# Kernel optimization log

Hardware: AMD Instinct MI355X
Metric: run time of the kernel (lower is better)

The kernel has to match this reference:

```python
import jax, jax.numpy as jnp
import numpy as np

NH, NKV, HD = 16, 8, 128  # heads, kv heads, head dim
N_REP = NH // NKV
EPS = 1e-06
K_MASK = float(jnp.finfo(jnp.bfloat16).min)
SCALE = HD ** -0.5


def _rms_norm(x, w):
    xf = x.astype(jnp.float32)
    rms = jnp.sqrt(jnp.mean(xf * xf, axis=-1, keepdims=True) + EPS)
    return (xf / rms * w).astype(x.dtype)


def _rotate_half(x):
    x1, x2 = jnp.split(x, 2, axis=-1)
    return jnp.concatenate([-x2, x1], axis=-1)


def setup_inputs() -> dict:
    key = jax.random.key(0)
    ks = jax.random.split(key, 5)
    B, S, H = 1, 2048, 2048
    hidden_states = jax.random.normal(ks[0], (B, S, H), jnp.float32)
    # real RoPE tables (duplicated-half layout), theta = 5e6
    pos = jnp.arange(S, dtype=jnp.float32)
    inv_freq = 1.0 / (5_000_000.0 ** (jnp.arange(0, HD, 2, dtype=jnp.float32) / HD))
    ang = pos[:, None] * inv_freq[None, :]            # (S, HD/2)
    emb = jnp.concatenate([ang, ang], axis=-1)[None]  # (1, S, HD)
    cos, sin = jnp.cos(emb), jnp.sin(emb)
    attention_mask = jnp.tril(jnp.ones((S, S), bool))[None, None]  # causal (1,1,S,S)
    sc = 0.02
    wq = jax.random.normal(ks[1], (H, NH * HD), jnp.float32) * sc
    wk = jax.random.normal(ks[2], (H, NKV * HD), jnp.float32) * sc
    wv = jax.random.normal(ks[3], (H, NKV * HD), jnp.float32) * sc
    wo = jax.random.normal(ks[4], (NH * HD, H), jnp.float32) * sc
    q_norm_w = jnp.ones((HD,), jnp.float32)
    k_norm_w = jnp.ones((HD,), jnp.float32)
    return {"hidden_states": hidden_states, "cos": cos, "sin": sin,
            "attention_mask": attention_mask, "wq": wq, "wk": wk, "wv": wv,
            "wo": wo, "q_norm_w": q_norm_w, "k_norm_w": k_norm_w}


def reference(hidden_states, cos, sin, attention_mask, wq, wk, wv, wo, q_norm_w, k_norm_w):
    B, S, H = hidden_states.shape
    q = (hidden_states @ wq).reshape(B, S, NH, HD)
    k = (hidden_states @ wk).reshape(B, S, NKV, HD)
    v = (hidden_states @ wv).reshape(B, S, NKV, HD)
    q = _rms_norm(q, q_norm_w)
    k = _rms_norm(k, k_norm_w)
    c = cos[:, :, None, :]
    s = sin[:, :, None, :]
    q = q * c + _rotate_half(q) * s
    k = k * c + _rotate_half(k) * s
    # GQA: group q heads by kv head; same math as jnp.repeat + matmul
    qg = q.reshape(B, S, NKV, N_REP, HD)
    scores = jnp.einsum('bqgrd,bkgd->bgrqk', qg, k) * SCALE  # (B,NKV,N_REP,S,S)
    scores = jnp.where(attention_mask[:, :, None], scores, K_MASK)
    attn = jax.nn.softmax(scores.astype(jnp.float32), axis=-1).astype(q.dtype)
    out = jnp.einsum('bgrqk,bkgd->bqgrd', attn, v)            # (B,S,NKV,N_REP,HD)
    out = out.reshape(B, S, NH * HD)
    return out @ wo
```

## Files before the change

### kernel.cpp

```cpp
#include <hip/hip_runtime.h>
#include <hip/hip_bf16.h>
#include <stdint.h>

typedef _Float16 half8 __attribute__((ext_vector_type(8)));
typedef _Float16 half4 __attribute__((ext_vector_type(4)));
typedef float f32x4 __attribute__((ext_vector_type(4)));

#define MFMA16(A, B, C) __builtin_amdgcn_mfma_f32_16x16x32_f16(A, B, C, 0, 0, 0)

static constexpr int Sdim = 2048;
static constexpr int NH = 16;
static constexpr int NKV = 8;
static constexpr int HD = 128;
static constexpr float ATT_SCALE = 0.08838834764831845f;
static constexpr float S0 = 4.0f;

__device__ __forceinline__ void async_copy16(const _Float16* g, _Float16* l) {
  auto gp = reinterpret_cast<const __attribute__((address_space(1))) uint32_t*>(
      reinterpret_cast<uintptr_t>(g));
  auto lp = reinterpret_cast<__attribute__((address_space(3))) uint32_t*>(
      reinterpret_cast<uintptr_t>(l));
  __builtin_amdgcn_global_load_lds(gp, lp, 16, 0, 0);
}

__global__ __launch_bounds__(256) void xconv(const float* __restrict__ X,
                                             _Float16* __restrict__ Xh) {
  int i = (blockIdx.x * 256 + threadIdx.x) * 4;
  float4 v = *(const float4*)(X + i);
  half4 h = {(_Float16)v.x, (_Float16)v.y, (_Float16)v.z, (_Float16)v.w};
  *(half4*)(Xh + i) = h;
}

__global__ __launch_bounds__(256) void wtrans_all(const float* __restrict__ wq,
                                                  const float* __restrict__ wk,
                                                  const float* __restrict__ wv,
                                                  const float* __restrict__ wo,
                                                  _Float16* __restrict__ wqT,
                                                  _Float16* __restrict__ wkT,
                                                  _Float16* __restrict__ wvT,
                                                  _Float16* __restrict__ woT) {
  const float* W;
  _Float16* WT;
  int N;
  switch (blockIdx.z) {
    case 0: W = wq; WT = wqT; N = 2048; break;
    case 1: W = wk; WT = wkT; N = 1024; break;
    case 2: W = wv; WT = wvT; N = 1024; break;
    default: W = wo; WT = woT; N = 2048; break;
  }
  if ((int)blockIdx.x * 64 >= N) return;
  const int K = 2048;
  __shared__ __align__(16) float tile[64][68];
  int n0 = blockIdx.x * 64, k0 = blockIdx.y * 64;
  int t = threadIdx.x;
  int c = (t & 15) * 4;
  int rb = t >> 4;
  for (int p = 0; p < 4; ++p) {
    int k = p * 16 + rb;
    *(float4*)&tile[k][c] = *(const float4*)(W + (size_t)(k0 + k) * N + n0 + c);
  }
  __syncthreads();
  int n = t >> 2;
  int kc = (t & 3) * 16;
  half8 o0, o1;
  for (int i = 0; i < 8; ++i) {
    o0[i] = (_Float16)tile[kc + i][n];
    o1[i] = (_Float16)tile[kc + 8 + i][n];
  }
  _Float16* dst = WT + (size_t)(n0 + n) * K + k0 + kc;
  *(half8*)dst = o0;
  *(half8*)(dst + 8) = o1;
}

template <int NI>
__device__ __forceinline__ void stage64(const _Float16* __restrict__ src, size_t stride,
                                        int k0, _Float16* lds, int w, int lane) {
  for (int ii = 0; ii < NI; ++ii) {
    int i = w * NI + ii;
    int row = i * 8 + (lane >> 3);
    int c = (lane & 7) ^ (row & 7);
    async_copy16(src + (size_t)row * stride + k0 + c * 8, lds + i * 512);
  }
}

__device__ __forceinline__ int frag_off(int row, int ks, int quad, int col) {
  return row * 64 + (((ks << 2) | quad) ^ (col & 7)) * 8;
}

__global__ __launch_bounds__(256, 2) void gemm_qkv(const _Float16* __restrict__ Xh,
                                                   const _Float16* __restrict__ wqT,
                                                   const _Float16* __restrict__ wkT,
                                                   const _Float16* __restrict__ wvT,
                                                   _Float16* __restrict__ Q,
                                                   _Float16* __restrict__ K,
                                                   _Float16* __restrict__ Vt) {
  __shared__ __align__(16) _Float16 As[2][128 * 64];
  __shared__ __align__(16) _Float16 Bs[2][128 * 64];
  int bx = blockIdx.x, m0 = blockIdx.y * 128;
  const _Float16* BT;
  _Float16* outp;
  int n0, Nst;
  bool vt;
  if (bx < 16)      { BT = wqT; outp = Q;  n0 = bx * 128;        vt = false; Nst = 2048; }
  else if (bx < 24) { BT = wkT; outp = K;  n0 = (bx - 16) * 128; vt = false; Nst = 1024; }
  else              { BT = wvT; outp = Vt; n0 = (bx - 24) * 128; vt = true;  Nst = 2048; }
  int t = threadIdx.x, lane = t & 63, w = t >> 6;
  int col = lane & 15, quad = lane >> 4;
  int wm = (w & 1) * 64, wn = (w >> 1) * 64;
  const _Float16* Ap = Xh + (size_t)m0 * 2048;
  const _Float16* Bp = BT + (size_t)n0 * 2048;
  f32x4 acc[4][4] = {};
  stage64<4>(Ap, 2048, 0, As[0], w, lane);
  stage64<4>(Bp, 2048, 0, Bs[0], w, lane);
#pragma unroll 1
  for (int it = 0; it < 32; ++it) {
    int c = it & 1;
    if (it + 1 < 32) {
      stage64<4>(Ap, 2048, (it + 1) * 64, As[c ^ 1], w, lane);
      stage64<4>(Bp, 2048, (it + 1) * 64, Bs[c ^ 1], w, lane);
      asm volatile("s_waitcnt vmcnt(8)" ::: "memory");
    } else {
      asm volatile("s_waitcnt vmcnt(0)" ::: "memory");
    }
    __builtin_amdgcn_sched_barrier(0);
    __builtin_amdgcn_s_barrier();
    __builtin_amdgcn_sched_barrier(0);
    half8 af[4][2], bf[4][2];
    for (int i = 0; i < 4; ++i)
      for (int ks = 0; ks < 2; ++ks) {
        af[i][ks] = *(const half8*)(As[c] + frag_off(wm + i * 16 + col, ks, quad, col));
        bf[i][ks] = *(const half8*)(Bs[c] + frag_off(wn + i * 16 + col, ks, quad, col));
      }
    __builtin_amdgcn_s_setprio(1);
    if (!vt) {
      for (int ks = 0; ks < 2; ++ks)
        for (int i = 0; i < 4; ++i)
          for (int j = 0; j < 4; ++j)
            acc[i][j] = MFMA16(bf[j][ks], af[i][ks], acc[i][j]);
    } else {
      for (int ks = 0; ks < 2; ++ks)
        for (int i = 0; i < 4; ++i)
          for (int j = 0; j < 4; ++j)
            acc[i][j] = MFMA16(af[i][ks], bf[j][ks], acc[i][j]);
    }
    __builtin_amdgcn_s_setprio(0);
    __builtin_amdgcn_sched_barrier(0);
    __builtin_amdgcn_s_barrier();
    __builtin_amdgcn_sched_barrier(0);
  }
  if (!vt) {
    for (int i = 0; i < 4; ++i)
      for (int j = 0; j < 4; ++j) {
        int m = m0 + wm + i * 16 + col;
        int n = n0 + wn + j * 16 + quad * 4;
        half4 hv = {(_Float16)acc[i][j][0], (_Float16)acc[i][j][1],
                    (_Float16)acc[i][j][2], (_Float16)acc[i][j][3]};
        *(half4*)(outp + (size_t)m * Nst + n) = hv;
      }
  } else {
    for (int i = 0; i < 4; ++i)
      for (int j = 0; j < 4; ++j) {
        int n = n0 + wn + j * 16 + col;
        int mb = m0 + wm + i * 16 + quad * 4;
        half4 hv = {(_Float16)acc[i][j][0], (_Float16)acc[i][j][1],
                    (_Float16)acc[i][j][2], (_Float16)acc[i][j][3]};
        *(half4*)(outp + (size_t)n * Sdim + mb) = hv;
      }
  }
}

__global__ __launch_bounds__(256, 2) void gemm_o(const _Float16* __restrict__ A,
                                                 const _Float16* __restrict__ BT,
                                                 float* __restrict__ C) {
  __shared__ __align__(16) _Float16 As[2][64 * 64];
  __shared__ __align__(16) _Float16 Bs[2][128 * 64];
  int m0 = blockIdx.y * 64, n0 = blockIdx.x * 128;
  int t = threadIdx.x, lane = t & 63, w = t >> 6;
  int col = lane & 15, quad = lane >> 4;
  int wm = (w & 1) * 32, wn = (w >> 1) * 64;
  const _Float16* Ap = A + (size_t)m0 * 2048;
  const _Float16* Bp = BT + (size_t)n0 * 2048;
  f32x4 acc[2][4] = {};
  stage64<2>(Ap, 2048, 0, As[0], w, lane);
  stage64<4>(Bp, 2048, 0, Bs[0], w, lane);
#pragma unroll 1
  for (int it = 0; it < 32; ++it) {
    int c = it & 1;
    if (it + 1 < 32) {
      stage64<2>(Ap, 2048, (it + 1) * 64, As[c ^ 1], w, lane);
      stage64<4>(Bp, 2048, (it + 1) * 64, Bs[c ^ 1], w, lane);
      asm volatile("s_waitcnt vmcnt(6)" ::: "memory");
    } else {
      asm volatile("s_waitcnt vmcnt(0)" ::: "memory");
    }
    __builtin_amdgcn_sched_barrier(0);
    __builtin_amdgcn_s_barrier();
    __builtin_amdgcn_sched_barrier(0);
    half8 af[2][2], bf[4][2];
    for (int ks = 0; ks < 2; ++ks) {
      for (int i = 0; i < 2; ++i)
        af[i][ks] = *(const half8*)(As[c] + frag_off(wm + i * 16 + col, ks, quad, col));
      for (int j = 0; j < 4; ++j)
        bf[j][ks] = *(const half8*)(Bs[c] + frag_off(wn + j * 16 + col, ks, quad, col));
    }
    __builtin_amdgcn_s_setprio(1);
    for (int ks = 0; ks < 2; ++ks)
      for (int i = 0; i < 2; ++i)
        for (int j = 0; j < 4; ++j)
          acc[i][j] = MFMA16(bf[j][ks], af[i][ks], acc[i][j]);
    __builtin_amdgcn_s_setprio(0);
    __builtin_amdgcn_sched_barrier(0);
    __builtin_amdgcn_s_barrier();
    __builtin_amdgcn_sched_barrier(0);
  }
  for (int i = 0; i < 2; ++i)
    for (int j = 0; j < 4; ++j) {
      int m = m0 + wm + i * 16 + col;
      int n = n0 + wn + j * 16 + quad * 4;
      *(f32x4*)(C + (size_t)m * 2048 + n) = acc[i][j];
    }
}

__global__ __launch_bounds__(256) void rmsrope_all(const _Float16* __restrict__ Qraw,
                                                   const _Float16* __restrict__ Kraw,
                                                   _Float16* __restrict__ Qn,
                                                   _Float16* __restrict__ Kn,
                                                   const float* __restrict__ cs,
                                                   const float* __restrict__ sn,
                                                   const float* __restrict__ qw,
                                                   const float* __restrict__ kw) {
  int w = threadIdx.x >> 6, lane = threadIdx.x & 63;
  int gw = blockIdx.x * 4 + w;
  const _Float16* src;
  _Float16* dst;
  const float* nw;
  int m, h, nh;
  float scale;
  if (gw < Sdim * NH) {
    m = gw >> 4; h = gw & 15; nh = NH; src = Qraw; dst = Qn; nw = qw; scale = ATT_SCALE;
  } else {
    int g2 = gw - Sdim * NH;
    m = g2 >> 3; h = g2 & 7; nh = NKV; src = Kraw; dst = Kn; nw = kw; scale = 1.0f;
  }
  const _Float16* p = src + (size_t)m * nh * HD + h * HD;
  float x0 = (float)p[lane], x1 = (float)p[lane + 64];
  float ss = x0 * x0 + x1 * x1;
#pragma unroll
  for (int o = 32; o > 0; o >>= 1) ss += __shfl_xor(ss, o);
  float inv = rsqrtf(ss * (1.0f / 128.0f) + 1e-6f);
  float n0v = x0 * inv * nw[lane], n1v = x1 * inv * nw[lane + 64];
  float c0 = cs[m * HD + lane], c1 = cs[m * HD + lane + 64];
  float s0 = sn[m * HD + lane], s1 = sn[m * HD + lane + 64];
  _Float16* q = dst + (size_t)m * nh * HD + h * HD;
  q[lane] = (_Float16)((n0v * c0 - n1v * s0) * scale);
  q[lane + 64] = (_Float16)((n1v * c1 + n0v * s1) * scale);
}

__device__ __forceinline__ void attn_pair(const half8* qf0, const half8* qf1,
                                          f32x4* O0, f32x4* O1, float* li0, float* li1,
                                          const _Float16* Ksb, const _Float16* Vsb,
                                          _Float16* Psw0, _Float16* Psw1, bool mask0,
                                          int col, int quad, int w) {
  f32x4 Sc0[4], Sc1[4];
  __builtin_amdgcn_s_setprio(1);
  for (int nt = 0; nt < 4; ++nt) {
    f32x4 a0 = {}, a1 = {};
    for (int kc = 0; kc < 4; ++kc) {
      half8 b = *(const half8*)(Ksb + (nt * 16 + col) * 128 + ((4 * kc + quad) ^ col) * 8);
      a0 = MFMA16(qf0[kc], b, a0);
      a1 = MFMA16(qf1[kc], b, a1);
    }
    Sc0[nt] = a0;
    Sc1[nt] = a1;
  }
  __builtin_amdgcn_s_setprio(0);
  if (mask0) {
    for (int nt = 0; nt < 4; ++nt)
      for (int r = 0; r < 4; ++r)
        if ((nt * 16 + col) > (w * 16 + quad * 4 + r)) Sc0[nt][r] = -1e4f;
  }
  for (int nt = 0; nt < 4; ++nt)
    for (int r = 0; r < 4; ++r) {
      float p0 = __expf(Sc0[nt][r] - S0);
      float p1 = __expf(Sc1[nt][r] - S0);
      Sc0[nt][r] = p0;
      li0[r] += p0;
      Sc1[nt][r] = p1;
      li1[r] += p1;
    }
  for (int nt = 0; nt < 4; ++nt)
    for (int r = 0; r < 4; ++r) {
      int q = quad * 4 + r;
      int off = q * 64 + (((2 * nt + (col >> 3)) ^ (q & 7)) * 8) + (col & 7);
      Psw0[off] = (_Float16)Sc0[nt][r];
      Psw1[off] = (_Float16)Sc1[nt][r];
    }
  __builtin_amdgcn_s_setprio(1);
  for (int c2 = 0; c2 < 2; ++c2) {
    int aoff = col * 64 + (((4 * c2 + quad) ^ (col & 7)) * 8);
    half8 ap0 = *(const half8*)(Psw0 + aoff);
    half8 ap1 = *(const half8*)(Psw1 + aoff);
    for (int nt = 0; nt < 8; ++nt) {
      half8 bv = *(const half8*)(Vsb + (nt * 16 + col) * 64 +
                                 (((4 * c2 + quad) ^ (col & 7)) * 8));
      O0[nt] = MFMA16(ap0, bv, O0[nt]);
      O1[nt] = MFMA16(ap1, bv, O1[nt]);
    }
  }
  __builtin_amdgcn_s_setprio(0);
}

__device__ __forceinline__ void attn_tile(const half8* qf, f32x4* O, float* li,
                                          const _Float16* Ksb, const _Float16* Vsb,
                                          _Float16* Psw, bool domask,
                                          int col, int quad, int w) {
  f32x4 Sc[4];
  __builtin_amdgcn_s_setprio(1);
  for (int nt = 0; nt < 4; ++nt) {
    f32x4 a = {};
    for (int kc = 0; kc < 4; ++kc) {
      half8 b = *(const half8*)(Ksb + (nt * 16 + col) * 128 + ((4 * kc + quad) ^ col) * 8);
      a = MFMA16(qf[kc], b, a);
    }
    Sc[nt] = a;
  }
  __builtin_amdgcn_s_setprio(0);
  if (domask) {
    for (int nt = 0; nt < 4; ++nt)
      for (int r = 0; r < 4; ++r)
        if ((nt * 16 + col) > (w * 16 + quad * 4 + r)) Sc[nt][r] = -1e4f;
  }
  for (int nt = 0; nt < 4; ++nt)
    for (int r = 0; r < 4; ++r) {
      float pv = __expf(Sc[nt][r] - S0);
      Sc[nt][r] = pv;
      li[r] += pv;
    }
  for (int nt = 0; nt < 4; ++nt)
    for (int r = 0; r < 4; ++r) {
      int q = quad * 4 + r;
      Psw[q * 64 + (((2 * nt + (col >> 3)) ^ (q & 7)) * 8) + (col & 7)] =
          (_Float16)Sc[nt][r];
    }
  __builtin_amdgcn_s_setprio(1);
  for (int c2 = 0; c2 < 2; ++c2) {
    half8 ap = *(const half8*)(Psw + col * 64 + (((4 * c2 + quad) ^ (col & 7)) * 8));
    for (int nt = 0; nt < 8; ++nt) {
      half8 bv = *(const half8*)(Vsb + (nt * 16 + col) * 64 +
                                 (((4 * c2 + quad) ^ (col & 7)) * 8));
      O[nt] = MFMA16(ap, bv, O[nt]);
    }
  }
  __builtin_amdgcn_s_setprio(0);
}

__global__ __launch_bounds__(256, 2) void fattn(const _Float16* __restrict__ Qn,
                                                const _Float16* __restrict__ Kn,
                                                const _Float16* __restrict__ Vt,
                                                _Float16* __restrict__ Op01,
                                                _Float16* __restrict__ Op2,
                                                float* __restrict__ lp) {
  __shared__ __align__(16) _Float16 Ks[2][64 * 128];
  __shared__ __align__(16) _Float16 Vs[2][128 * 64];
  __shared__ __align__(16) _Float16 Ps[2][4 * 1024];
  int f = blockIdx.x;
  int Wk = (f & 7) * 96 + (f >> 3);
  int xb = Wk & 15, h = (Wk >> 4) & 15, s = Wk >> 8;
  int p = 15 - xb;
  int g = h >> 1;
  int qb0 = 2 * p, qb1 = 2 * p + 1;
  int t = threadIdx.x, lane = t & 63, w = t >> 6;
  int col = lane & 15, quad = lane >> 4;
  _Float16* Psw0 = Ps[0] + w * 1024;
  _Float16* Psw1 = Ps[1] + w * 1024;
  _Float16* op = (s == 2) ? Op2 : Op01 + (size_t)s * Sdim * (NH * HD);
  float* lpp = lp + (size_t)s * NH * Sdim + (size_t)h * Sdim;

  auto stageKV = [&](int b, int kt) {
    for (int ii = 0; ii < 4; ++ii) {
      int i = w * 4 + ii;
      int krow = i * 4 + (lane >> 4);
      int kc = (lane & 15) ^ (krow & 15);
      async_copy16(Kn + (size_t)(kt * 64 + krow) * (NKV * HD) + g * HD + kc * 8,
                   Ks[b] + i * 512);
      int vrow = i * 8 + (lane >> 3);
      int vc = (lane & 7) ^ (vrow & 7);
      async_copy16(Vt + (size_t)(g * HD + vrow) * Sdim + kt * 64 + vc * 8,
                   Vs[b] + i * 512);
    }
  };

  half8 qf0[4], qf1[4];
  {
    int qr0 = qb0 * 64 + w * 16 + col;
    int qr1 = qb1 * 64 + w * 16 + col;
    for (int kc = 0; kc < 4; ++kc) {
      qf0[kc] = *(const half8*)(Qn + (size_t)qr0 * (NH * HD) + h * HD + kc * 32 + quad * 8);
      qf1[kc] = *(const half8*)(Qn + (size_t)qr1 * (NH * HD) + h * HD + kc * 32 + quad * 8);
    }
  }
  f32x4 O0[8] = {}, O1[8] = {};
  float li0[4] = {}, li1[4] = {};

  int ntt = (qb1 >= s) ? ((qb1 - s) / 3 + 1) : 0;
  if (ntt > 0) {
    stageKV(0, s);
#pragma unroll 1
    for (int it = 0; it < ntt; ++it) {
      int kt = s + it * 3;
      int c = it & 1;
      if (it + 1 < ntt) {
        stageKV(c ^ 1, kt + 3);
        asm volatile("s_waitcnt vmcnt(8)" ::: "memory");
      } else {
        asm volatile("s_waitcnt vmcnt(0)" ::: "memory");
      }
      __builtin_amdgcn_sched_barrier(0);
      __builtin_amdgcn_s_barrier();
      __builtin_amdgcn_sched_barrier(0);
      const _Float16* Kb = Ks[c];
      const _Float16* Vb = Vs[c];
      if (kt <= qb0) {
        attn_pair(qf0, qf1, O0, O1, li0, li1, Kb, Vb, Psw0, Psw1, kt == qb0,
                  col, quad, w);
      } else {
        attn_tile(qf1, O1, li1, Kb, Vb, Psw0, kt == qb1, col, quad, w);
      }
      __builtin_amdgcn_sched_barrier(0);
      __builtin_amdgcn_s_barrier();
      __builtin_amdgcn_sched_barrier(0);
    }
  }

  auto finish = [&](f32x4* O, float* li, int qb) {
    for (int r = 0; r < 4; ++r) {
      float sm = li[r];
      sm += __shfl_xor(sm, 1);
      sm += __shfl_xor(sm, 2);
      sm += __shfl_xor(sm, 4);
      sm += __shfl_xor(sm, 8);
      li[r] = sm;
    }
    for (int ntile = 0; ntile < 8; ++ntile)
      for (int r = 0; r < 4; ++r) {
        int m = qb * 64 + w * 16 + quad * 4 + r;
        op[(size_t)m * (NH * HD) + h * HD + ntile * 16 + col] = (_Float16)O[ntile][r];
      }
    if (col == 0)
      for (int r = 0; r < 4; ++r) lpp[qb * 64 + w * 16 + quad * 4 + r] = li[r];
  };
  finish(O0, li0, qb0);
  finish(O1, li1, qb1);
}

__global__ __launch_bounds__(256) void merge(const _Float16* __restrict__ Op01,
                                             const _Float16* __restrict__ Op2,
                                             const float* __restrict__ lp,
                                             _Float16* __restrict__ attn) {
  int m = blockIdx.x, t = threadIdx.x;
  int h = t >> 4, d0 = (t & 15) * 8;
  size_t off = (size_t)m * (NH * HD) + h * HD + d0;
  half8 o0 = *(const half8*)(Op01 + off);
  half8 o1 = *(const half8*)(Op01 + (size_t)Sdim * NH * HD + off);
  half8 o2 = *(const half8*)(Op2 + off);
  float l = lp[(size_t)h * Sdim + m] +
            lp[(size_t)NH * Sdim + (size_t)h * Sdim + m] +
            lp[2 * (size_t)NH * Sdim + (size_t)h * Sdim + m];
  float ri = 1.0f / l;
  half8 o;
  for (int i = 0; i < 8; ++i)
    o[i] = (_Float16)(((float)o0[i] + (float)o1[i] + (float)o2[i]) * ri);
  *(half8*)(attn + off) = o;
}

extern "C" void kernel_launch(void* const* d_in, const int* in_sizes, int n_in,
                              void* d_out, int out_size, void* d_ws, size_t ws_size,
                              hipStream_t stream) {
  (void)in_sizes; (void)n_in; (void)out_size; (void)ws_size;
  const float* X  = (const float*)d_in[0];
  const float* cs = (const float*)d_in[1];
  const float* sn = (const float*)d_in[2];
  const float* wq = (const float*)d_in[4];
  const float* wk = (const float*)d_in[5];
  const float* wv = (const float*)d_in[6];
  const float* wo = (const float*)d_in[7];
  const float* qw = (const float*)d_in[8];
  const float* kw = (const float*)d_in[9];
  char* ws = (char*)d_ws;
  const size_t MB = 1024 * 1024;
  _Float16* wqT  = (_Float16*)(ws + 0 * MB);
  _Float16* wkT  = (_Float16*)(ws + 8 * MB);
  _Float16* wvT  = (_Float16*)(ws + 12 * MB);
  _Float16* woT  = (_Float16*)(ws + 16 * MB);
  _Float16* Xh   = (_Float16*)(ws + 24 * MB);
  _Float16* Qraw = (_Float16*)(ws + 32 * MB);
  _Float16* Kraw = (_Float16*)(ws + 40 * MB);
  _Float16* Vt   = (_Float16*)(ws + 44 * MB);
  _Float16* Qn   = (_Float16*)(ws + 48 * MB);
  _Float16* Kn   = (_Float16*)(ws + 56 * MB);
  float*    lp   = (float*)(ws + 60 * MB);
  _Float16* Op01 = wqT;
  _Float16* Op2  = Xh;
  _Float16* attn = Qraw;
  float* out = (float*)d_out;

  xconv<<<4096, 256, 0, stream>>>(X, Xh);
  wtrans_all<<<dim3(32, 32, 4), 256, 0, stream>>>(wq, wk, wv, wo, wqT, wkT, wvT, woT);

  gemm_qkv<<<dim3(32, 16), 256, 0, stream>>>(Xh, wqT, wkT, wvT, Qraw, Kraw, Vt);

  rmsrope_all<<<(Sdim * NH + Sdim * NKV) / 4, 256, 0, stream>>>(Qraw, Kraw, Qn, Kn,
                                                                cs, sn, qw, kw);

  fattn<<<768, 256, 0, stream>>>(Qn, Kn, Vt, Op01, Op2, lp);
  merge<<<2048, 256, 0, stream>>>(Op01, Op2, lp, attn);

  gemm_o<<<dim3(16, 32), 256, 0, stream>>>(attn, woT, out);
}
```

Baseline: 287.1 us.

## Pair symmetric causal query blocks and split KV into two interleaved slices

Changes the flash-attention work split. Each block now pairs query block xb with 31-xb, which balances the causal work, and the KV range is split into two interleaved slices instead of three. The grid drops from 768 to 512 blocks, and the merge kernel sums two partials instead of three. The exp and P store loops are also fused. The gains are better load balance and less partial-output traffic, at the cost of fewer blocks, which may lower occupancy.

```diff
diff --git a/kernel.cpp b/kernel.cpp
--- a/kernel.cpp
+++ b/kernel.cpp
@@ -256,11 +256,12 @@
   q[lane + 64] = (_Float16)((n1v * c1 + n0v * s1) * scale);
 }
 
-__device__ __forceinline__ void attn_pair(const half8* qf0, const half8* qf1,
-                                          f32x4* O0, f32x4* O1, float* li0, float* li1,
-                                          const _Float16* Ksb, const _Float16* Vsb,
-                                          _Float16* Psw0, _Float16* Psw1, bool mask0,
-                                          int col, int quad, int w) {
+__device__ __forceinline__ void attn_pair_fused(const half8* qf0, const half8* qf1,
+                                                f32x4* O0, f32x4* O1,
+                                                float* li0, float* li1,
+                                                const _Float16* Ksb, const _Float16* Vsb,
+                                                _Float16* Psw0, _Float16* Psw1,
+                                                bool mask1, int col, int quad, int w) {
   f32x4 Sc0[4], Sc1[4];
   __builtin_amdgcn_s_setprio(1);
   for (int nt = 0; nt < 4; ++nt) {
@@ -274,26 +275,21 @@
     Sc1[nt] = a1;
   }
   __builtin_amdgcn_s_setprio(0);
-  if (mask0) {
+  if (mask1) {
     for (int nt = 0; nt < 4; ++nt)
       for (int r = 0; r < 4; ++r)
-        if ((nt * 16 + col) > (w * 16 + quad * 4 + r)) Sc0[nt][r] = -1e4f;
+        if ((nt * 16 + col) > (w * 16 + quad * 4 + r)) Sc1[nt][r] = -1e4f;
   }
   for (int nt = 0; nt < 4; ++nt)
     for (int r = 0; r < 4; ++r) {
       float p0 = __expf(Sc0[nt][r] - S0);
       float p1 = __expf(Sc1[nt][r] - S0);
-      Sc0[nt][r] = p0;
       li0[r] += p0;
-      Sc1[nt][r] = p1;
       li1[r] += p1;
-    }
-  for (int nt = 0; nt < 4; ++nt)
-    for (int r = 0; r < 4; ++r) {
       int q = quad * 4 + r;
       int off = q * 64 + (((2 * nt + (col >> 3)) ^ (q & 7)) * 8) + (col & 7);
-      Psw0[off] = (_Float16)Sc0[nt][r];
-      Psw1[off] = (_Float16)Sc1[nt][r];
+      Psw0[off] = (_Float16)p0;
+      Psw1[off] = (_Float16)p1;
     }
   __builtin_amdgcn_s_setprio(1);
   for (int c2 = 0; c2 < 2; ++c2) {
@@ -358,22 +354,20 @@
                                                 const _Float16* __restrict__ Kn,
                                                 const _Float16* __restrict__ Vt,
                                                 _Float16* __restrict__ Op01,
-                                                _Float16* __restrict__ Op2,
                                                 float* __restrict__ lp) {
   __shared__ __align__(16) _Float16 Ks[2][64 * 128];
   __shared__ __align__(16) _Float16 Vs[2][128 * 64];
   __shared__ __align__(16) _Float16 Ps[2][4 * 1024];
   int f = blockIdx.x;
-  int Wk = (f & 7) * 96 + (f >> 3);
+  int Wk = (f & 7) * 64 + (f >> 3);
   int xb = Wk & 15, h = (Wk >> 4) & 15, s = Wk >> 8;
-  int p = 15 - xb;
   int g = h >> 1;
-  int qb0 = 2 * p, qb1 = 2 * p + 1;
+  int qb0 = 31 - xb, qb1 = xb;
   int t = threadIdx.x, lane = t & 63, w = t >> 6;
   int col = lane & 15, quad = lane >> 4;
   _Float16* Psw0 = Ps[0] + w * 1024;
   _Float16* Psw1 = Ps[1] + w * 1024;
-  _Float16* op = (s == 2) ? Op2 : Op01 + (size_t)s * Sdim * (NH * HD);
+  _Float16* op = Op01 + (size_t)s * Sdim * (NH * HD);
   float* lpp = lp + (size_t)s * NH * Sdim + (size_t)h * Sdim;
 
   auto stageKV = [&](int b, int kt) {
@@ -402,34 +396,32 @@
   f32x4 O0[8] = {}, O1[8] = {};
   float li0[4] = {}, li1[4] = {};
 
-  int ntt = (qb1 >= s) ? ((qb1 - s) / 3 + 1) : 0;
-  if (ntt > 0) {
-    stageKV(0, s);
+  int nt = (qb0 - s) / 2 + 1;
+  stageKV(0, s);
 #pragma unroll 1
-    for (int it = 0; it < ntt; ++it) {
-      int kt = s + it * 3;
-      int c = it & 1;
-      if (it + 1 < ntt) {
-        stageKV(c ^ 1, kt + 3);
-        asm volatile("s_waitcnt vmcnt(8)" ::: "memory");
-      } else {
-        asm volatile("s_waitcnt vmcnt(0)" ::: "memory");
-      }
-      __builtin_amdgcn_sched_barrier(0);
-      __builtin_amdgcn_s_barrier();
-      __builtin_amdgcn_sched_barrier(0);
-      const _Float16* Kb = Ks[c];
-      const _Float16* Vb = Vs[c];
-      if (kt <= qb0) {
-        attn_pair(qf0, qf1, O0, O1, li0, li1, Kb, Vb, Psw0, Psw1, kt == qb0,
-                  col, quad, w);
-      } else {
-        attn_tile(qf1, O1, li1, Kb, Vb, Psw0, kt == qb1, col, quad, w);
-      }
-      __builtin_amdgcn_sched_barrier(0);
-      __builtin_amdgcn_s_barrier();
-      __builtin_amdgcn_sched_barrier(0);
-    }
+  for (int it = 0; it < nt; ++it) {
+    int kt = s + it * 2;
+    int c = it & 1;
+    if (it + 1 < nt) {
+      stageKV(c ^ 1, kt + 2);
+      asm volatile("s_waitcnt vmcnt(8)" ::: "memory");
+    } else {
+      asm volatile("s_waitcnt vmcnt(0)" ::: "memory");
+    }
+    __builtin_amdgcn_sched_barrier(0);
+    __builtin_amdgcn_s_barrier();
+    __builtin_amdgcn_sched_barrier(0);
+    const _Float16* Kb = Ks[c];
+    const _Float16* Vb = Vs[c];
+    if (kt <= qb1) {
+      attn_pair_fused(qf0, qf1, O0, O1, li0, li1, Kb, Vb, Psw0, Psw1, kt == qb1,
+                      col, quad, w);
+    } else {
+      attn_tile(qf0, O0, li0, Kb, Vb, Psw0, kt == qb0, col, quad, w);
+    }
+    __builtin_amdgcn_sched_barrier(0);
+    __builtin_amdgcn_s_barrier();
+    __builtin_amdgcn_sched_barrier(0);
   }
 
   auto finish = [&](f32x4* O, float* li, int qb) {
@@ -454,7 +446,6 @@
 }
 
 __global__ __launch_bounds__(256) void merge(const _Float16* __restrict__ Op01,
-                                             const _Float16* __restrict__ Op2,
                                              const float* __restrict__ lp,
                                              _Float16* __restrict__ attn) {
   int m = blockIdx.x, t = threadIdx.x;
@@ -462,14 +453,12 @@
   size_t off = (size_t)m * (NH * HD) + h * HD + d0;
   half8 o0 = *(const half8*)(Op01 + off);
   half8 o1 = *(const half8*)(Op01 + (size_t)Sdim * NH * HD + off);
-  half8 o2 = *(const half8*)(Op2 + off);
   float l = lp[(size_t)h * Sdim + m] +
-            lp[(size_t)NH * Sdim + (size_t)h * Sdim + m] +
-            lp[2 * (size_t)NH * Sdim + (size_t)h * Sdim + m];
+            lp[(size_t)NH * Sdim + (size_t)h * Sdim + m];
   float ri = 1.0f / l;
   half8 o;
   for (int i = 0; i < 8; ++i)
-    o[i] = (_Float16)(((float)o0[i] + (float)o1[i] + (float)o2[i]) * ri);
+    o[i] = (_Float16)(((float)o0[i] + (float)o1[i]) * ri);
   *(half8*)(attn + off) = o;
 }
 
@@ -500,7 +489,6 @@
   _Float16* Kn   = (_Float16*)(ws + 56 * MB);
   float*    lp   = (float*)(ws + 60 * MB);
   _Float16* Op01 = wqT;
-  _Float16* Op2  = Xh;
   _Float16* attn = Qraw;
   float* out = (float*)d_out;
 
@@ -512,8 +500,8 @@
   rmsrope_all<<<(Sdim * NH + Sdim * NKV) / 4, 256, 0, stream>>>(Qraw, Kraw, Qn, Kn,
                                                                 cs, sn, qw, kw);
 
-  fattn<<<768, 256, 0, stream>>>(Qn, Kn, Vt, Op01, Op2, lp);
-  merge<<<2048, 256, 0, stream>>>(Op01, Op2, lp, attn);
+  fattn<<<512, 256, 0, stream>>>(Qn, Kn, Vt, Op01, lp);
+  merge<<<2048, 256, 0, stream>>>(Op01, lp, attn);
 
   gemm_o<<<dim3(16, 32), 256, 0, stream>>>(attn, woT, out);
 }
```

Result: no change. 286.5 us (-0.2%).
